# Kernel optimization log

Measured on AMD Instinct MI355X. Metric: run time of the kernel, lower is better.

## Reference

```python
import jax, jax.numpy as jnp
import numpy as np
from jax import lax

N, D, BATCH = 8192, 256, 64


def setup_inputs() -> dict:
    key = jax.random.key(0)
    V = jax.random.normal(key, (N, D), dtype=jnp.float32)
    V = V / jnp.linalg.norm(V, axis=1, keepdims=True)  # cosine = raw dot product
    return {
        "V": V,
        "cos_threshold": jnp.array([0.25], dtype=jnp.float32),
        "batch_size": BATCH,
    }


def reference(V, cos_threshold, batch_size):
    """Faithful port of Embeddings._fast_predict: batched cosine-sim thresholding
    followed by a sequential transitive merge of group ids.

    Returns group_ids [N] int32 (the clustering result; the torch code wraps this
    into a Matcher object, which is pure python bookkeeping).
    """
    n, d = V.shape
    B = int(batch_size)
    n_batches = n // B
    thr = cos_threshold[0]
    j_idx = jnp.arange(n, dtype=jnp.int32)
    group_init = jnp.arange(n, dtype=jnp.int32)

    def outer(gids, batch_start):
        # group ids as of the start of this batch (torch computes batch_matched
        # with these, but reads live group_ids inside the row loop via views)
        g0 = gids
        Vb = lax.dynamic_slice(V, (batch_start, 0), (B, d))        # [B, D]
        sims = Vb @ V.T                                            # [B, N]
        g0_i = lax.dynamic_slice(g0, (batch_start,), (B,))         # [B]
        jmask = j_idx > batch_start                                # j_slice = batch_start+1 .. N
        mask = (sims >= thr) & jmask[None, :] & (g0_i[:, None] != g0[None, :])  # [B, N]

        def inner(g, inp):
            k, row = inp
            gi = g[batch_start + k]  # live group id of row i (torch g_i is a view)
            # isin(group_ids, matched_groups): flag[label]=1 if any matched j has
            # current group label == label, then gather back through g
            flag = jnp.zeros(n, jnp.int32).at[g].max(row.astype(jnp.int32))
            g = jnp.where(flag[g] > 0, gi, g)
            return g, None

        gids, _ = lax.scan(inner, gids, (jnp.arange(B, dtype=jnp.int32), mask))
        return gids, None

    starts = jnp.arange(n_batches, dtype=jnp.int32) * B
    gids, _ = lax.scan(outer, group_init, starts)
    return gids
```

## Files before the change

### kernel.cpp

```cpp
#include <hip/hip_runtime.h>
#include <stdint.h>

#define NPTS 8192
#define DIM  256
#define CAP  32768
#define LDSE 8192
#define BAND 2.0e-3f

typedef _Float16 f16x8  __attribute__((ext_vector_type(8)));
typedef float    f32x16 __attribute__((ext_vector_type(16)));


__global__ __launch_bounds__(256) void convert_kernel(
        const float* __restrict__ V, _Float16* __restrict__ Vh,
        unsigned* __restrict__ ctr) {
    if (blockIdx.x == 0 && threadIdx.x == 0) { ctr[0] = 0u; ctr[1] = 0u; }
    size_t t = (size_t)blockIdx.x * 256 + threadIdx.x;
    const float4* src = reinterpret_cast<const float4*>(V) + t * 2;
    float4 v0 = src[0], v1 = src[1];
    f16x8 h;
    h[0] = (_Float16)v0.x; h[1] = (_Float16)v0.y;
    h[2] = (_Float16)v0.z; h[3] = (_Float16)v0.w;
    h[4] = (_Float16)v1.x; h[5] = (_Float16)v1.y;
    h[6] = (_Float16)v1.z; h[7] = (_Float16)v1.w;
    *reinterpret_cast<f16x8*>(Vh + t * 8) = h;
}

__global__ void init_count(unsigned* ctr) {
    if (threadIdx.x == 0) { ctr[0] = 0u; ctr[1] = 0u; }
}

__device__ __forceinline__ void gload_lds16(const void* g, void* l) {
    __builtin_amdgcn_global_load_lds(
        (const __attribute__((address_space(1))) void*)g,
        (__attribute__((address_space(3))) void*)l, 16, 0, 0);
}

__global__ __launch_bounds__(256, 4) void edge_mfma(
        const _Float16* __restrict__ Vh,
        const float* __restrict__ thr_p,
        unsigned* __restrict__ ctr,
        unsigned* __restrict__ edges,
        unsigned* __restrict__ cand) {
    int t = blockIdx.x;
    int bi = (int)(64.5f - sqrtf(64.5f * 64.5f - 2.0f * (float)t));
    while (bi * 64 - (bi * (bi - 1)) / 2 > t) --bi;
    while ((bi + 1) * 64 - ((bi + 1) * bi) / 2 <= t) ++bi;
    int bj = bi + (t - (bi * 64 - (bi * (bi - 1)) / 2));

    __shared__ _Float16 L[2 * 128 * 64];

    const float thr = thr_p[0];
    const float hi = thr + BAND, lo = thr - BAND;
    const int tid  = threadIdx.x;
    const int lane = tid & 63;
    const int wid  = tid >> 6;
    const int wr = wid >> 1, wc = wid & 1;
    const int i0 = bi * 128, j0 = bj * 128;

    f32x16 acc[2][2];
#pragma unroll
    for (int a = 0; a < 2; ++a)
#pragma unroll
        for (int b = 0; b < 2; ++b) acc[a][b] = 0.0f;

    const int row_l = lane >> 3;
    const int bphys = lane & 7;
    const int l31 = lane & 31, g = lane >> 5, l7 = lane & 7;

    for (int kc = 0; kc < DIM; kc += 64) {
#pragma unroll
        for (int q = 0; q < 8; ++q) {
            const int qq  = wid * 8 + q;
            const int arr = qq >> 4;
            const int ins = qq & 15;
            const int row = ins * 8 + row_l;
            const int blk = bphys ^ row_l;
            const int grow = (arr ? j0 : i0) + row;
            gload_lds16(Vh + ((size_t)grow * DIM + kc + blk * 8),
                        &L[arr * 8192 + ins * 512]);
        }
        __syncthreads();

#pragma unroll
        for (int s = 0; s < 4; ++s) {
            const int xa = (((s * 2 + g) ^ l7) << 3);
            f16x8 ah[2], bh[2];
#pragma unroll
            for (int a = 0; a < 2; ++a) {
                ah[a] = *(const f16x8*)&L[(wr * 64 + a * 32 + l31) * 64 + xa];
                bh[a] = *(const f16x8*)&L[8192 + (wc * 64 + a * 32 + l31) * 64 + xa];
            }
#pragma unroll
            for (int a = 0; a < 2; ++a)
#pragma unroll
                for (int b = 0; b < 2; ++b)
                    acc[a][b] = __builtin_amdgcn_mfma_f32_32x32x16_f16(
                        ah[a], bh[b], acc[a][b], 0, 0, 0);
        }
        __syncthreads();
    }

    const int rbase = 4 * (lane >> 5);
#pragma unroll
    for (int a = 0; a < 2; ++a)
#pragma unroll
        for (int b = 0; b < 2; ++b)
#pragma unroll
            for (int reg = 0; reg < 16; ++reg) {
                float sim = acc[a][b][reg];
                int row = (reg & 3) + 8 * (reg >> 2) + rbase;
                int i = i0 + wr * 64 + a * 32 + row;
                int j = j0 + wc * 64 + b * 32 + l31;
                if (j > i && sim >= lo) {
                    unsigned key = ((unsigned)i << 13) | (unsigned)j;
                    if (sim >= hi) {
                        unsigned p = atomicAdd(&ctr[0], 1u);
                        if (p < CAP) edges[p] = key;
                    } else {
                        unsigned p = atomicAdd(&ctr[1], 1u);
                        if (p < CAP) cand[p] = key;
                    }
                }
            }
}

__global__ __launch_bounds__(256) void edge_kernel(
        const float* __restrict__ V,
        const float* __restrict__ thr_p,
        unsigned*    __restrict__ ctr,
        unsigned*    __restrict__ edges) {
    const int bi = blockIdx.y, bj = blockIdx.x;
    if (bj < bi) return;

    __shared__ float As[128 * 32];
    __shared__ float Bs[128 * 32];

    const float thr = thr_p[0];
    const int tid = threadIdx.x;
    const int tx = tid & 15, ty = tid >> 4;
    const int i0 = bi * 128, j0 = bj * 128;

    float acc[8][8];
#pragma unroll
    for (int r = 0; r < 8; ++r)
#pragma unroll
        for (int c = 0; c < 8; ++c) acc[r][c] = 0.f;

    const int srow = tid >> 3, sq = tid & 7;

    for (int kc = 0; kc < DIM; kc += 32) {
#pragma unroll
        for (int p = 0; p < 4; ++p) {
            int row = srow + 32 * p;
            float4 va = *reinterpret_cast<const float4*>(
                &V[(size_t)(i0 + row) * DIM + kc + sq * 4]);
            float4 vb = *reinterpret_cast<const float4*>(
                &V[(size_t)(j0 + row) * DIM + kc + sq * 4]);
            int w = row * 32 + ((sq ^ ((row >> 3) & 7)) << 2);
            *reinterpret_cast<float4*>(&As[w]) = va;
            *reinterpret_cast<float4*>(&Bs[w]) = vb;
        }
        __syncthreads();
#pragma unroll
        for (int k4 = 0; k4 < 8; ++k4) {
            const float* pA = &As[(ty * 8) * 32 + ((k4 ^ (ty & 7)) << 2)];
            const float* pB = &Bs[(tx * 8) * 32 + ((k4 ^ (tx & 7)) << 2)];
            float4 a[8], b[8];
#pragma unroll
            for (int r = 0; r < 8; ++r)
                a[r] = *reinterpret_cast<const float4*>(&pA[r * 32]);
#pragma unroll
            for (int c = 0; c < 8; ++c)
                b[c] = *reinterpret_cast<const float4*>(&pB[c * 32]);
#pragma unroll
            for (int r = 0; r < 8; ++r)
#pragma unroll
                for (int c = 0; c < 8; ++c) {
                    acc[r][c] = fmaf(a[r].x, b[c].x, acc[r][c]);
                    acc[r][c] = fmaf(a[r].y, b[c].y, acc[r][c]);
                    acc[r][c] = fmaf(a[r].z, b[c].z, acc[r][c]);
                    acc[r][c] = fmaf(a[r].w, b[c].w, acc[r][c]);
                }
        }
        __syncthreads();
    }
#pragma unroll
    for (int r = 0; r < 8; ++r)
#pragma unroll
        for (int c = 0; c < 8; ++c) {
            int i = i0 + ty * 8 + r;
            int j = j0 + tx * 8 + c;
            if (j > i && acc[r][c] >= thr) {
                unsigned p = atomicAdd(&ctr[0], 1u);
                if (p < CAP) edges[p] = ((unsigned)i << 13) | (unsigned)j;
            }
        }
}

__global__ __launch_bounds__(1024) void uf_kernel(
        const unsigned* __restrict__ ctr,
        const unsigned* __restrict__ edges,
        const unsigned* __restrict__ cand,
        const float* __restrict__ V,
        const float* __restrict__ thr_p,
        int* __restrict__ out) {
    __shared__ int      par[NPTS];
    __shared__ unsigned slot[NPTS];
    __shared__ unsigned sedge[LDSE];
    __shared__ unsigned nE_s, nRem_s;

    const int tid  = threadIdx.x;
    const int lane = tid & 63;
    const int wv   = tid >> 6;

    unsigned EC = ctr[0]; if (EC > LDSE) EC = LDSE;
    unsigned CC = ctr[1]; if (CC > CAP)  CC = CAP;

    for (int t = tid; t < NPTS; t += 1024) { par[t] = t; slot[t] = 0xFFFFFFFFu; }
    if (tid == 0) nE_s = EC;
    __syncthreads();

    for (unsigned e = tid; e < EC; e += 1024) sedge[e] = edges[e];

    const float thr = thr_p[0];
    for (unsigned c = wv; c < CC; c += 16) {
        unsigned key = cand[c];
        int i = (int)(key >> 13), j = (int)(key & 8191u);
        const float* vi = V + (size_t)i * DIM;
        const float* vj = V + (size_t)j * DIM;
        double sum = 0.0;
        for (int k = lane; k < DIM; k += 64)
            sum += (double)vi[k] * (double)vj[k];
#pragma unroll
        for (int d = 32; d; d >>= 1) sum += __shfl_down(sum, d);
        if (lane == 0 && sum >= (double)thr) {
            unsigned p = atomicAdd(&nE_s, 1u);
            if (p < LDSE) sedge[p] = key;
        }
    }
    __syncthreads();

    unsigned nE = nE_s; if (nE > LDSE) nE = LDSE;
    if (tid == 0) nRem_s = nE;
    __syncthreads();

    volatile int* vpar = par;

    while (true) {
        unsigned rem = nRem_s;
        if (rem == 0) break;
        for (unsigned e = tid; e < nE; e += 1024) {
            unsigned key = sedge[e];
            if (key & 0x80000000u) continue;
            int ri = (int)(key >> 13), rj = (int)(key & 8191u);
            int p;
            while ((p = vpar[ri]) != ri) ri = p;
            while ((p = vpar[rj]) != rj) rj = p;
            atomicMin(&slot[ri], key);
            atomicMin(&slot[rj], key);
        }
        __syncthreads();
        for (unsigned e = tid; e < nE; e += 1024) {
            unsigned key = sedge[e];
            if (key & 0x80000000u) continue;
            int i = (int)(key >> 13), j = (int)(key & 8191u);
            int ri = i, rj = j, p;
            while ((p = vpar[ri]) != ri) ri = p;
            while ((p = vpar[rj]) != rj) rj = p;
            if (slot[ri] == key && slot[rj] == key) {
                if (ri != rj) { par[rj] = ri; par[i] = ri; par[j] = ri; }
                sedge[e] = key | 0x80000000u;
                atomicSub(&nRem_s, 1u);
            }
        }
        __syncthreads();
        for (int t = tid; t < NPTS; t += 1024) slot[t] = 0xFFFFFFFFu;
        __syncthreads();
    }

    for (int t = tid; t < NPTS; t += 1024) {
        int r = t, p;
        while ((p = par[r]) != r) r = p;
        out[t] = r;
    }
}

extern "C" void kernel_launch(void* const* d_in, const int* in_sizes, int n_in,
                              void* d_out, int out_size, void* d_ws, size_t ws_size,
                              hipStream_t stream) {
    const float* V     = (const float*)d_in[0];
    const float* thr_p = (const float*)d_in[1];

    unsigned* ctr   = (unsigned*)d_ws;
    unsigned* edges = (unsigned*)((char*)d_ws + 64);
    unsigned* cand  = (unsigned*)((char*)d_ws + (256u << 10));
    int*      out   = (int*)d_out;

    const size_t vhOff = 1u << 20;
    const size_t vN    = (size_t)NPTS * DIM;
    const size_t need  = vhOff + vN * sizeof(_Float16) + 65536;

    if (ws_size >= need) {
        _Float16* Vh = (_Float16*)((char*)d_ws + vhOff);
        hipLaunchKernelGGL(convert_kernel, dim3(1024), dim3(256), 0, stream,
                           V, Vh, ctr);
        hipLaunchKernelGGL(edge_mfma, dim3(2080), dim3(256), 0, stream,
                           Vh, thr_p, ctr, edges, cand);
    } else {
        hipLaunchKernelGGL(init_count, dim3(1), dim3(64), 0, stream, ctr);
        hipLaunchKernelGGL(edge_kernel, dim3(64, 64), dim3(256), 0, stream,
                           V, thr_p, ctr, edges);
    }
    hipLaunchKernelGGL(uf_kernel, dim3(1), dim3(1024), 0, stream,
                       ctr, edges, cand, V, thr_p, out);
}
```

Measured before the change: 120.1 us.

## Verify borderline candidates inside edge tiles and double-buffer union-find slots

Borderline similarity pairs are no longer sent to a global candidate list for fp64 recheck in the single-block union-find kernel. Each edge tile now collects them in shared memory and rechecks them in fp64 itself, spreading that serial work across the whole grid. The union-find loop alternates between two slot arrays and uses __syncthreads_count for termination, which removes one barrier and the shared remaining-edge counter per round. The per-tile candidate buffer is capped at 256, so overflow would silently drop candidates, and the edge tiles pay extra latency for the fp32 global loads.

```diff
diff --git a/kernel.cpp b/kernel.cpp
--- a/kernel.cpp
+++ b/kernel.cpp
@@ -5,6 +5,7 @@
 #define DIM  256
 #define CAP  32768
 #define LDSE 8192
+#define IBCAP 256
 #define BAND 2.0e-3f
 
 typedef _Float16 f16x8  __attribute__((ext_vector_type(8)));
@@ -38,10 +39,10 @@
 
 __global__ __launch_bounds__(256, 4) void edge_mfma(
         const _Float16* __restrict__ Vh,
+        const float* __restrict__ V,
         const float* __restrict__ thr_p,
         unsigned* __restrict__ ctr,
-        unsigned* __restrict__ edges,
-        unsigned* __restrict__ cand) {
+        unsigned* __restrict__ edges) {
     int t = blockIdx.x;
     int bi = (int)(64.5f - sqrtf(64.5f * 64.5f - 2.0f * (float)t));
     while (bi * 64 - (bi * (bi - 1)) / 2 > t) --bi;
@@ -49,6 +50,8 @@
     int bj = bi + (t - (bi * 64 - (bi * (bi - 1)) / 2));
 
     __shared__ _Float16 L[2 * 128 * 64];
+    __shared__ unsigned ibl[IBCAP];
+    __shared__ unsigned ibn;
 
     const float thr = thr_p[0];
     const float hi = thr + BAND, lo = thr - BAND;
@@ -57,6 +60,8 @@
     const int wid  = tid >> 6;
     const int wr = wid >> 1, wc = wid & 1;
     const int i0 = bi * 128, j0 = bj * 128;
+
+    if (tid == 0) ibn = 0u;
 
     f32x16 acc[2][2];
 #pragma unroll
@@ -118,11 +123,32 @@
                         unsigned p = atomicAdd(&ctr[0], 1u);
                         if (p < CAP) edges[p] = key;
                     } else {
-                        unsigned p = atomicAdd(&ctr[1], 1u);
-                        if (p < CAP) cand[p] = key;
+                        unsigned p = atomicAdd(&ibn, 1u);
+                        if (p < IBCAP) ibl[p] = key;
                     }
                 }
             }
+    __syncthreads();
+
+    unsigned nib = ibn; if (nib > IBCAP) nib = IBCAP;
+    const double thrd = (double)thr;
+    for (unsigned q = tid; q < nib; q += 256) {
+        unsigned key = ibl[q];
+        int i = (int)(key >> 13), j = (int)(key & 8191u);
+        const float4* a4 = reinterpret_cast<const float4*>(V + (size_t)i * DIM);
+        const float4* b4 = reinterpret_cast<const float4*>(V + (size_t)j * DIM);
+        double s = 0.0;
+#pragma unroll 4
+        for (int k = 0; k < DIM / 4; ++k) {
+            float4 x = a4[k], y = b4[k];
+            s += (double)x.x * y.x + (double)x.y * y.y
+               + (double)x.z * y.z + (double)x.w * y.w;
+        }
+        if (s >= thrd) {
+            unsigned p = atomicAdd(&ctr[0], 1u);
+            if (p < CAP) edges[p] = key;
+        }
+    }
 }
 
 __global__ __launch_bounds__(256) void edge_kernel(
@@ -201,82 +227,57 @@
 __global__ __launch_bounds__(1024) void uf_kernel(
         const unsigned* __restrict__ ctr,
         const unsigned* __restrict__ edges,
-        const unsigned* __restrict__ cand,
-        const float* __restrict__ V,
-        const float* __restrict__ thr_p,
         int* __restrict__ out) {
     __shared__ int      par[NPTS];
-    __shared__ unsigned slot[NPTS];
+    __shared__ unsigned slotA[NPTS];
+    __shared__ unsigned slotB[NPTS];
     __shared__ unsigned sedge[LDSE];
-    __shared__ unsigned nE_s, nRem_s;
-
-    const int tid  = threadIdx.x;
-    const int lane = tid & 63;
-    const int wv   = tid >> 6;
+
+    const int tid = threadIdx.x;
 
     unsigned EC = ctr[0]; if (EC > LDSE) EC = LDSE;
-    unsigned CC = ctr[1]; if (CC > CAP)  CC = CAP;
-
-    for (int t = tid; t < NPTS; t += 1024) { par[t] = t; slot[t] = 0xFFFFFFFFu; }
-    if (tid == 0) nE_s = EC;
+
+    for (int t = tid; t < NPTS; t += 1024) {
+        par[t] = t; slotA[t] = 0xFFFFFFFFu; slotB[t] = 0xFFFFFFFFu;
+    }
+    for (unsigned e = tid; e < EC; e += 1024) sedge[e] = edges[e];
     __syncthreads();
 
-    for (unsigned e = tid; e < EC; e += 1024) sedge[e] = edges[e];
-
-    const float thr = thr_p[0];
-    for (unsigned c = wv; c < CC; c += 16) {
-        unsigned key = cand[c];
-        int i = (int)(key >> 13), j = (int)(key & 8191u);
-        const float* vi = V + (size_t)i * DIM;
-        const float* vj = V + (size_t)j * DIM;
-        double sum = 0.0;
-        for (int k = lane; k < DIM; k += 64)
-            sum += (double)vi[k] * (double)vj[k];
-#pragma unroll
-        for (int d = 32; d; d >>= 1) sum += __shfl_down(sum, d);
-        if (lane == 0 && sum >= (double)thr) {
-            unsigned p = atomicAdd(&nE_s, 1u);
-            if (p < LDSE) sedge[p] = key;
-        }
-    }
-    __syncthreads();
-
-    unsigned nE = nE_s; if (nE > LDSE) nE = LDSE;
-    if (tid == 0) nRem_s = nE;
-    __syncthreads();
-
     volatile int* vpar = par;
 
-    while (true) {
-        unsigned rem = nRem_s;
-        if (rem == 0) break;
-        for (unsigned e = tid; e < nE; e += 1024) {
+    for (int round = 0;; ++round) {
+        unsigned* S = (round & 1) ? slotB : slotA;
+        unsigned* T = (round & 1) ? slotA : slotB;
+
+        for (unsigned e = tid; e < EC; e += 1024) {
             unsigned key = sedge[e];
             if (key & 0x80000000u) continue;
             int ri = (int)(key >> 13), rj = (int)(key & 8191u);
             int p;
             while ((p = vpar[ri]) != ri) ri = p;
             while ((p = vpar[rj]) != rj) rj = p;
-            atomicMin(&slot[ri], key);
-            atomicMin(&slot[rj], key);
-        }
-        __syncthreads();
-        for (unsigned e = tid; e < nE; e += 1024) {
+            atomicMin(&S[ri], key);
+            atomicMin(&S[rj], key);
+        }
+        __syncthreads();
+
+        int mylive = 0;
+        for (unsigned e = tid; e < EC; e += 1024) {
             unsigned key = sedge[e];
             if (key & 0x80000000u) continue;
             int i = (int)(key >> 13), j = (int)(key & 8191u);
             int ri = i, rj = j, p;
             while ((p = vpar[ri]) != ri) ri = p;
             while ((p = vpar[rj]) != rj) rj = p;
-            if (slot[ri] == key && slot[rj] == key) {
+            if (S[ri] == key && S[rj] == key) {
                 if (ri != rj) { par[rj] = ri; par[i] = ri; par[j] = ri; }
                 sedge[e] = key | 0x80000000u;
-                atomicSub(&nRem_s, 1u);
+            } else {
+                mylive = 1;
             }
         }
-        __syncthreads();
-        for (int t = tid; t < NPTS; t += 1024) slot[t] = 0xFFFFFFFFu;
-        __syncthreads();
+        for (int t = tid; t < NPTS; t += 1024) T[t] = 0xFFFFFFFFu;
+        if (__syncthreads_count(mylive) == 0) break;
     }
 
     for (int t = tid; t < NPTS; t += 1024) {
@@ -294,7 +295,6 @@
 
     unsigned* ctr   = (unsigned*)d_ws;
     unsigned* edges = (unsigned*)((char*)d_ws + 64);
-    unsigned* cand  = (unsigned*)((char*)d_ws + (256u << 10));
     int*      out   = (int*)d_out;
 
     const size_t vhOff = 1u << 20;
@@ -306,12 +306,12 @@
         hipLaunchKernelGGL(convert_kernel, dim3(1024), dim3(256), 0, stream,
                            V, Vh, ctr);
         hipLaunchKernelGGL(edge_mfma, dim3(2080), dim3(256), 0, stream,
-                           Vh, thr_p, ctr, edges, cand);
+                           Vh, V, thr_p, ctr, edges);
     } else {
         hipLaunchKernelGGL(init_count, dim3(1), dim3(64), 0, stream, ctr);
         hipLaunchKernelGGL(edge_kernel, dim3(64, 64), dim3(256), 0, stream,
                            V, thr_p, ctr, edges);
     }
     hipLaunchKernelGGL(uf_kernel, dim3(1), dim3(1024), 0, stream,
-                       ctr, edges, cand, V, thr_p, out);
-}
+                       ctr, edges, out);
+}
```

Result: faster. 99.68 us (-17.0%).
